# Kernel optimization log

Measured on AMD Instinct MI355X. Metric: run time of the kernel, lower is better.

Reference implementation:

```python
import jax, jax.numpy as jnp
import numpy as np

K = 3          # kernel size
STRIDE = 1
PAD = 1
DIL = 1
K2 = K * K


def setup_inputs() -> dict:
    key = jax.random.key(0)
    ks = jax.random.split(key, 5)
    B, Cin, Cout, H, W = 8, 128, 128, 64, 64
    x = jax.random.normal(ks[0], (B, Cin, H, W), jnp.float32)
    # conv_offset_mask: Conv2d(Cin, 3*dg*K*K=27, 3x3). Original inits to zero;
    # use small random weights so offsets are nonzero sub-pixel shifts.
    w_off = jax.random.normal(ks[1], (3 * K2, Cin, K, K), jnp.float32) * 0.05
    b_off = jax.random.normal(ks[2], (3 * K2,), jnp.float32) * 0.1
    weight = jax.random.normal(ks[3], (Cout, Cin, K, K), jnp.float32) / np.sqrt(Cin * K2)
    bias = jax.random.normal(ks[4], (Cout,), jnp.float32) * 0.1
    return dict(x=x, w_off=w_off, b_off=b_off, weight=weight, bias=bias)


def _conv(x, w, b):
    y = jax.lax.conv_general_dilated(
        x, w, (STRIDE, STRIDE), [(PAD, PAD), (PAD, PAD)],
        dimension_numbers=('NCHW', 'OIHW', 'NCHW'))
    return y + b[None, :, None, None]


def _sample_one(xb, pyb, pxb, mb):
    Cin, Hin, Win = xb.shape
    y0 = jnp.floor(pyb)
    x0 = jnp.floor(pxb)
    wy = pyb - y0   # fractional weights
    wx = pxb - x0
    y0i = y0.astype(jnp.int32)
    x0i = x0.astype(jnp.int32)
    xf = xb.reshape(Cin, -1)

    def g(yi, xi):
        valid = ((yi >= 0) & (yi < Hin) & (xi >= 0) & (xi < Win)).astype(xb.dtype)
        idx = jnp.clip(yi, 0, Hin - 1) * Win + jnp.clip(xi, 0, Win - 1)
        return xf[:, idx] * valid[None]   # [Cin,K2,Ho,Wo]

    v = (g(y0i, x0i) * ((1 - wy) * (1 - wx))[None]
         + g(y0i, x0i + 1) * ((1 - wy) * wx)[None]
         + g(y0i + 1, x0i) * (wy * (1 - wx))[None]
         + g(y0i + 1, x0i + 1) * (wy * wx)[None])
    return v * mb[None]   # modulated columns [Cin,K2,Ho,Wo]


def reference(x, w_off, b_off, weight, bias):
    B, Cin, Hin, Win = x.shape
    Cout = weight.shape[0]
    om = _conv(x, w_off, b_off)                 # [B, 3*K2, Ho, Wo]
    dy = om[:, :K2]
    dx = om[:, K2:2 * K2]
    m = jax.nn.sigmoid(om[:, 2 * K2:])          # modulation mask
    Ho, Wo = dy.shape[2], dy.shape[3]
    kh = jnp.repeat(jnp.arange(K), K)           # [K2] kernel row per tap
    kw = jnp.tile(jnp.arange(K), K)             # [K2] kernel col per tap
    grid_y = jnp.arange(Ho) * STRIDE - PAD
    grid_x = jnp.arange(Wo) * STRIDE - PAD
    py = dy + grid_y[None, None, :, None] + (kh * DIL)[None, :, None, None]
    px = dx + grid_x[None, None, None, :] + (kw * DIL)[None, :, None, None]
    cols = jax.vmap(_sample_one)(x, py, px, m)  # [B,Cin,K2,Ho,Wo]
    out = jnp.einsum('bckhw,ock->bohw', cols, weight.reshape(Cout, Cin, K2))
    return out + bias[None, :, None, None]
```

## Files before the change

kernel.cpp:

```cpp
#include <hip/hip_runtime.h>
#include <math.h>

#define BATCH 8
#define CIN   128
#define COUT  128
#define HH    64
#define WW    64
#define OC    27
#define KDIM  1152

typedef unsigned short u16;
typedef unsigned int   u32;
typedef __attribute__((ext_vector_type(8))) short bf16x8;
typedef __attribute__((ext_vector_type(4))) float f32x4;

__device__ __forceinline__ float b2f(u16 u) {
    return __uint_as_float((u32)u << 16);
}
__device__ __forceinline__ u16 f2b(float f) {
    u32 u = __float_as_uint(f);
    return (u16)((u + 0x7fffu + ((u >> 16) & 1u)) >> 16);
}
__device__ __forceinline__ float blo(u32 u) { return __uint_as_float(u << 16); }
__device__ __forceinline__ float bhi(u32 u) { return __uint_as_float(u & 0xffff0000u); }
__device__ __forceinline__ u32 cvtpk(float lo, float hi) {
    u32 r;
    asm("v_cvt_pk_bf16_f32 %0, %1, %2" : "=v"(r) : "v"(lo), "v"(hi));
    return r;
}

__device__ __forceinline__ int xswiz(int o, int K) { return (o & 7) * K + (o >> 3); }

__global__ __launch_bounds__(256) void k_prep(const float* __restrict__ x,
                                              const float* __restrict__ weight,
                                              const float* __restrict__ w_off,
                                              u16* __restrict__ xtb,
                                              u16* __restrict__ xlo,
                                              u16* __restrict__ wbf,
                                              u16* __restrict__ wop) {
    __shared__ float tile[64][65];
    int gbid = blockIdx.x;
    int t = threadIdx.x;
    if (gbid < 1024) {
        int bid = xswiz(gbid, 128);
        int b   = bid >> 7;
        int c0  = ((bid >> 6) & 1) << 6;
        int hw0 = (bid & 63) << 6;
        int ln  = t & 63;
        int cq  = t >> 6;
#pragma unroll
        for (int r = 0; r < 16; ++r) {
            int c_l = cq * 16 + r;
            tile[c_l][ln] = x[(((size_t)(b * CIN + c0 + c_l)) << 12) + hw0 + ln];
        }
        __syncthreads();
#pragma unroll
        for (int r = 0; r < 16; ++r) {
            int hw_w = cq * 16 + r;
            float v = tile[ln][hw_w];
            u16 hi = f2b(v);
            u16 lo = f2b(v - b2f(hi));
            size_t dst = ((size_t)(b << 12) + hw0 + hw_w) * 128 + c0 + ln;
            xtb[dst] = hi;
            xlo[dst] = lo;
        }
    } else if (gbid < 1600) {
        int tid = (gbid - 1024) * 256 + t;
        int j  = tid & 7;
        int l  = (tid >> 3) & 63;
        int ni = (tid >> 9) & 7;
        int s  = (tid >> 12) & 3;
        int t9 = tid >> 14;
        int co = ni * 16 + (l & 15);
        int ci = s * 32 + ((l >> 4) << 3) + j;
        wbf[tid] = f2b(weight[co * KDIM + ci * 9 + t9]);
    } else {
        int tid = (gbid - 1600) * 256 + t;
        int j   = tid & 7;
        int l   = (tid >> 3) & 63;
        int ni  = (tid >> 9) & 1;
        int sg  = (tid >> 10) & 3;
        int rest = tid >> 12;
        int t9  = rest % 9;
        int split = rest / 9;
        int co = ni * 16 + (l & 15);
        int ci = sg * 32 + ((l >> 4) << 3) + j;
        float val = (co < OC) ? w_off[co * KDIM + ci * 9 + t9] : 0.f;
        u16 hi = f2b(val);
        u16 lo = f2b(val - b2f(hi));
        wop[tid] = split ? lo : hi;
    }
}

__global__ __launch_bounds__(512, 4) void k_off_mfma(const u16* __restrict__ xtb,
                                                     const u16* __restrict__ xlo,
                                                     const u16* __restrict__ wop,
                                                     const float* __restrict__ b_off,
                                                     float* __restrict__ om) {
    __shared__ __align__(16) u16 Xh[3 * 66 * 64];
    __shared__ __align__(16) u16 Xl[3 * 66 * 64];
    __shared__ __align__(16) float red[4][32][16];

    const int t    = threadIdx.x;
    const int lb   = xswiz(blockIdx.x, 64);
    const int b    = lb >> 6;
    const int h    = lb & 63;
    const int tl   = t & 255;
    const int sgrp = t >> 8;
    const int l    = tl & 63;
    const int wv2  = tl >> 6;
    const int row0 = l & 15;
    const int kg   = l >> 4;

    f32x4 acc0 = {0.f, 0.f, 0.f, 0.f};
    f32x4 acc1 = {0.f, 0.f, 0.f, 0.f};

    bf16x8 vh_[4], vl_[4];
    const bf16x8 zero8 = {0, 0, 0, 0, 0, 0, 0, 0};

    auto stage_load = [&](int half) {
#pragma unroll
        for (int it = 0; it < 4; ++it) {
            int i = t + it * 512;
            vh_[it] = zero8;
            vl_[it] = zero8;
            if (i < 1584) {
                int row = i / 528;
                int rem = i - row * 528;
                int p = rem >> 3, q = rem & 7;
                int grow = h - 1 + row;
                int gw   = p - 1;
                if ((unsigned)grow < 64u && (unsigned)gw < 64u) {
                    size_t src = ((((size_t)b << 12) + (grow << 6) + gw) << 7) + half * 64 + q * 8;
                    vh_[it] = *(const bf16x8*)(xtb + src);
                    vl_[it] = *(const bf16x8*)(xlo + src);
                }
            }
        }
    };
    auto stage_store = [&]() {
#pragma unroll
        for (int it = 0; it < 4; ++it) {
            int i = t + it * 512;
            if (i < 1584) {
                int row = i / 528;
                int rem = i - row * 528;
                int p = rem >> 3, q = rem & 7;
                int dstb = ((row * 66 + p) << 7) + ((q ^ (p & 7)) << 4);
                *(bf16x8*)((char*)Xh + dstb) = vh_[it];
                *(bf16x8*)((char*)Xl + dstb) = vl_[it];
            }
        }
    };
    auto kloop = [&](int half) {
        for (int tap = 0; tap < 9; ++tap) {
            int kh = tap / 3, kw = tap - kh * 3;
            int p = wv2 * 16 + row0 + kw;
            int rowb = (kh * 66 + p) << 7;
            int q = sgrp * 4 + kg;
            int off = rowb + ((q ^ (p & 7)) << 4);
            bf16x8 ah = *(const bf16x8*)((const char*)Xh + off);
            bf16x8 al = *(const bf16x8*)((const char*)Xl + off);
            int sg = half * 2 + sgrp;
            const u16* B = wop + (((tap * 4 + sg)) << 10) + (l << 3);
            bf16x8 bh0 = *(const bf16x8*)(B);
            bf16x8 bh1 = *(const bf16x8*)(B + 512);
            bf16x8 bl0 = *(const bf16x8*)(B + 36864);
            bf16x8 bl1 = *(const bf16x8*)(B + 36864 + 512);
            acc0 = __builtin_amdgcn_mfma_f32_16x16x32_bf16(ah, bh0, acc0, 0, 0, 0);
            acc1 = __builtin_amdgcn_mfma_f32_16x16x32_bf16(ah, bh1, acc1, 0, 0, 0);
            acc0 = __builtin_amdgcn_mfma_f32_16x16x32_bf16(al, bh0, acc0, 0, 0, 0);
            acc1 = __builtin_amdgcn_mfma_f32_16x16x32_bf16(al, bh1, acc1, 0, 0, 0);
            acc0 = __builtin_amdgcn_mfma_f32_16x16x32_bf16(ah, bl0, acc0, 0, 0, 0);
            acc1 = __builtin_amdgcn_mfma_f32_16x16x32_bf16(ah, bl1, acc1, 0, 0, 0);
        }
    };

    stage_load(0);
    stage_store();
    __syncthreads();
    stage_load(1);
    kloop(0);
    __syncthreads();
    stage_store();
    __syncthreads();
    kloop(1);

    if (sgrp) {
        *(f32x4*)&red[wv2][row0][kg * 4]      = acc0;
        *(f32x4*)&red[wv2][row0 + 16][kg * 4] = acc1;
    }
    __syncthreads();
    if (!sgrp) {
        acc0 += *(const f32x4*)&red[wv2][row0][kg * 4];
        acc1 += *(const f32x4*)&red[wv2][row0 + 16][kg * 4];
        int wpx = wv2 * 16 + (kg << 2);
        int co0 = row0;
        {
            float bb = b_off[co0];
            float4 r = make_float4(acc0.x + bb, acc0.y + bb, acc0.z + bb, acc0.w + bb);
            *(float4*)(om + (((size_t)(b * OC + co0)) << 12) + (h << 6) + wpx) = r;
        }
        int co1 = co0 + 16;
        if (co1 < OC) {
            float bb = b_off[co1];
            float4 r = make_float4(acc1.x + bb, acc1.y + bb, acc1.z + bb, acc1.w + bb);
            if (co1 >= 18) {
                r.x = 1.f / (1.f + expf(-r.x));
                r.y = 1.f / (1.f + expf(-r.y));
                r.z = 1.f / (1.f + expf(-r.z));
                r.w = 1.f / (1.f + expf(-r.w));
            }
            *(float4*)(om + (((size_t)(b * OC + co1)) << 12) + (h << 6) + wpx) = r;
        }
    }
}

__global__ __launch_bounds__(512, 4) void k_sample_gemm(const u16* __restrict__ xtb,
                                                        const float* __restrict__ om,
                                                        const u16* __restrict__ wbf,
                                                        const float* __restrict__ bias,
                                                        float* __restrict__ out) {
    __shared__ __align__(16) u16 Abuf[2][64 * 128];
    __shared__ float w4[576][4];
    __shared__ int y0c[576], x0c[576], y1c[576], x1c[576];

    const int t  = threadIdx.x;
    const int lb = xswiz(blockIdx.x, 64);
    const int b  = lb >> 6;
    const int h  = lb & 63;

    for (int i = t; i < 576; i += 512) {
        int p  = i / 9;
        int tt = i - p * 9;
        const float* ob = om + ((size_t)b * OC) * 4096 + (h << 6) + p;
        float dy = ob[(size_t)tt << 12];
        float dx = ob[(size_t)(9 + tt) << 12];
        float m  = ob[(size_t)(18 + tt) << 12];
        float py = dy + (float)(h - 1 + tt / 3);
        float px = dx + (float)(p - 1 + tt % 3);
        float y0f = floorf(py), x0f = floorf(px);
        float wy = py - y0f, wx = px - x0f;
        int y0 = (int)y0f, x0 = (int)x0f;
        int y1 = y0 + 1,   x1 = x0 + 1;
        float vy0 = ((unsigned)y0 < 64u) ? 1.f : 0.f;
        float vy1 = ((unsigned)y1 < 64u) ? 1.f : 0.f;
        float vx0 = ((unsigned)x0 < 64u) ? 1.f : 0.f;
        float vx1 = ((unsigned)x1 < 64u) ? 1.f : 0.f;
        w4[i][0] = (1.f - wy) * (1.f - wx) * m * vy0 * vx0;
        w4[i][1] = (1.f - wy) * wx         * m * vy0 * vx1;
        w4[i][2] = wy         * (1.f - wx) * m * vy1 * vx0;
        w4[i][3] = wy         * wx         * m * vy1 * vx1;
        y0c[i] = min(max(y0, 0), 63);
        y1c[i] = min(max(y1, 0), 63);
        x0c[i] = min(max(x0, 0), 63);
        x1c[i] = min(max(x1, 0), 63);
    }
    __syncthreads();

    f32x4 acc[4][2];
#pragma unroll
    for (int pt = 0; pt < 4; ++pt)
#pragma unroll
        for (int nt = 0; nt < 2; ++nt) acc[pt][nt] = (f32x4){0.f, 0.f, 0.f, 0.f};

    const int grp  = t >> 8;
    const int tl   = t & 255;
    const int l    = tl & 63;
    const int wv2  = tl >> 6;
    const int row0 = l & 15;
    const int kg   = l >> 4;

    const int sp = tl >> 2;
    const int sc = tl & 3;
    const u16* xb = xtb + ((size_t)b << 19);

    uint4 g_[2][4];

    auto sample_load = [&](int tt) {
        int pi = sp * 9 + tt;
        int o00 = (((y0c[pi] << 6) | x0c[pi]) << 7) + grp * 64;
        int o01 = (((y0c[pi] << 6) | x1c[pi]) << 7) + grp * 64;
        int o10 = (((y1c[pi] << 6) | x0c[pi]) << 7) + grp * 64;
        int o11 = (((y1c[pi] << 6) | x1c[pi]) << 7) + grp * 64;
#pragma unroll
        for (int k = 0; k < 2; ++k) {
            int ch = k * 32 + sc * 8;
            g_[k][0] = *(const uint4*)(xb + o00 + ch);
            g_[k][1] = *(const uint4*)(xb + o01 + ch);
            g_[k][2] = *(const uint4*)(xb + o10 + ch);
            g_[k][3] = *(const uint4*)(xb + o11 + ch);
        }
    };

    auto sample_finish = [&](int tt, int buf) {
        int pi = sp * 9 + tt;
        float4 W = *(const float4*)(&w4[pi][0]);
        u16* dst = &Abuf[buf][0];
#pragma unroll
        for (int k = 0; k < 2; ++k) {
            uint4 a00 = g_[k][0], a01 = g_[k][1], a10 = g_[k][2], a11 = g_[k][3];
            uint4 ow;
            {
                float e0 = W.x * blo(a00.x) + W.y * blo(a01.x) + W.z * blo(a10.x) + W.w * blo(a11.x);
                float e1 = W.x * bhi(a00.x) + W.y * bhi(a01.x) + W.z * bhi(a10.x) + W.w * bhi(a11.x);
                ow.x = cvtpk(e0, e1);
            }
            {
                float e0 = W.x * blo(a00.y) + W.y * blo(a01.y) + W.z * blo(a10.y) + W.w * blo(a11.y);
                float e1 = W.x * bhi(a00.y) + W.y * bhi(a01.y) + W.z * bhi(a10.y) + W.w * bhi(a11.y);
                ow.y = cvtpk(e0, e1);
            }
            {
                float e0 = W.x * blo(a00.z) + W.y * blo(a01.z) + W.z * blo(a10.z) + W.w * blo(a11.z);
                float e1 = W.x * bhi(a00.z) + W.y * bhi(a01.z) + W.z * bhi(a10.z) + W.w * bhi(a11.z);
                ow.z = cvtpk(e0, e1);
            }
            {
                float e0 = W.x * blo(a00.w) + W.y * blo(a01.w) + W.z * blo(a10.w) + W.w * blo(a11.w);
                float e1 = W.x * bhi(a00.w) + W.y * bhi(a01.w) + W.z * bhi(a10.w) + W.w * bhi(a11.w);
                ow.w = cvtpk(e0, e1);
            }
            int q16 = (grp * 8 + k * 4 + sc) ^ (sp & 15);
            *(uint4*)((char*)dst + (sp << 8) + (q16 << 4)) = ow;
        }
    };

    auto domfma = [&](int t9, int buf) {
        const char* Ab = (const char*)&Abuf[buf][0];
#pragma unroll
        for (int shalf = 0; shalf < 2; ++shalf) {
            int s = grp * 2 + shalf;
            int q = s * 4 + kg;
            int sw = (q ^ row0) << 4;
            bf16x8 a[4];
#pragma unroll
            for (int pt = 0; pt < 4; ++pt)
                a[pt] = *(const bf16x8*)(Ab + ((pt * 16 + row0) << 8) + sw);
            const u16* B = wbf + ((size_t)t9 << 14) + (s << 12) + (wv2 << 10) + (l << 3);
            bf16x8 b0 = *(const bf16x8*)(B);
            bf16x8 b1 = *(const bf16x8*)(B + 512);
#pragma unroll
            for (int pt = 0; pt < 4; ++pt) {
                acc[pt][0] = __builtin_amdgcn_mfma_f32_16x16x32_bf16(a[pt], b0, acc[pt][0], 0, 0, 0);
                acc[pt][1] = __builtin_amdgcn_mfma_f32_16x16x32_bf16(a[pt], b1, acc[pt][1], 0, 0, 0);
            }
        }
    };

    sample_load(0);
    sample_finish(0, 0);
    __syncthreads();
    for (int tt = 0; tt < 9; ++tt) {
        if (tt < 8) sample_load(tt + 1);
        domfma(tt, tt & 1);
        if (tt < 8) sample_finish(tt + 1, (tt + 1) & 1);
        __syncthreads();
    }

    float* outs = (float*)&Abuf[0][0];
    if (grp) {
#pragma unroll
        for (int pt = 0; pt < 4; ++pt)
#pragma unroll
            for (int nt = 0; nt < 2; ++nt) {
                int co  = wv2 * 32 + nt * 16 + row0;
                int pxq = pt * 4 + kg;
                *(f32x4*)((char*)outs + (co << 8) + ((pxq ^ (co & 7)) << 4)) = acc[pt][nt];
            }
    }
    __syncthreads();
    if (!grp) {
#pragma unroll
        for (int pt = 0; pt < 4; ++pt)
#pragma unroll
            for (int nt = 0; nt < 2; ++nt) {
                int co  = wv2 * 32 + nt * 16 + row0;
                int pxq = pt * 4 + kg;
                char* ad = (char*)outs + (co << 8) + ((pxq ^ (co & 7)) << 4);
                f32x4 v = *(const f32x4*)ad;
                *(f32x4*)ad = v + acc[pt][nt];
            }
    }
    __syncthreads();
    {
        int co = t >> 2, qt = t & 3;
        float bb = bias[co];
        float* og = out + (((size_t)(b * COUT + co)) << 12) + (h << 6);
#pragma unroll
        for (int j = 0; j < 4; ++j) {
            int pxq = qt * 4 + j;
            f32x4 v = *(const f32x4*)((const char*)outs + (co << 8) + ((pxq ^ (co & 7)) << 4));
            float4 r = make_float4(v.x + bb, v.y + bb, v.z + bb, v.w + bb);
            *reinterpret_cast<float4*>(og + pxq * 4) = r;
        }
    }
}

extern "C" void kernel_launch(void* const* d_in, const int* in_sizes, int n_in,
                              void* d_out, int out_size, void* d_ws, size_t ws_size,
                              hipStream_t stream) {
    const float* x      = (const float*)d_in[0];
    const float* w_off  = (const float*)d_in[1];
    const float* b_off  = (const float*)d_in[2];
    const float* weight = (const float*)d_in[3];
    const float* bias   = (const float*)d_in[4];
    float* out = (float*)d_out;

    float* om  = (float*)d_ws;
    u16*   xtb = (u16*)(om + 884736);
    u16*   wbf = xtb + 4194304;
    u16*   wop = wbf + 147456;
    u16*   xlo = (u16*)d_out;

    k_prep<<<1888, 256, 0, stream>>>(x, weight, w_off, xtb, xlo, wbf, wop);
    k_off_mfma<<<512, 512, 0, stream>>>(xtb, xlo, wop, b_off, om);
    k_sample_gemm<<<512, 512, 0, stream>>>(xtb, om, wbf, bias, out);
}
```

Baseline: 56.31 us.

## Fuse offset conv into sample-GEMM kernel, computing hi/lo bf16 split on the fly

Merges the offset/mask convolution kernel into the deformable sampling GEMM kernel. The per-row offsets stay in shared memory instead of making a round trip through a global workspace. The offset conv now stages raw fp32 x rows into LDS and forms the bf16 hi/lo split per MFMA operand, so the prep kernel no longer writes the xlo array. This removes a kernel launch and the global traffic for om and xlo. In exchange it uses more LDS per block (about 72KB), which may reduce occupancy, and adds conversion ALU work inside the offset conv loop.

```diff
diff --git a/kernel.cpp b/kernel.cpp
--- a/kernel.cpp
+++ b/kernel.cpp
@@ -28,6 +28,11 @@
     asm("v_cvt_pk_bf16_f32 %0, %1, %2" : "=v"(r) : "v"(lo), "v"(hi));
     return r;
 }
+__device__ __forceinline__ bf16x8 pack8(u32 a, u32 b, u32 c, u32 d) {
+    union { u32 u[4]; bf16x8 v; } z;
+    z.u[0] = a; z.u[1] = b; z.u[2] = c; z.u[3] = d;
+    return z.v;
+}
 
 __device__ __forceinline__ int xswiz(int o, int K) { return (o & 7) * K + (o >> 3); }
 
@@ -35,7 +40,6 @@
                                               const float* __restrict__ weight,
                                               const float* __restrict__ w_off,
                                               u16* __restrict__ xtb,
-                                              u16* __restrict__ xlo,
                                               u16* __restrict__ wbf,
                                               u16* __restrict__ wop) {
     __shared__ float tile[64][65];
@@ -57,12 +61,7 @@
 #pragma unroll
         for (int r = 0; r < 16; ++r) {
             int hw_w = cq * 16 + r;
-            float v = tile[ln][hw_w];
-            u16 hi = f2b(v);
-            u16 lo = f2b(v - b2f(hi));
-            size_t dst = ((size_t)(b << 12) + hw0 + hw_w) * 128 + c0 + ln;
-            xtb[dst] = hi;
-            xlo[dst] = lo;
+            xtb[((size_t)(b << 12) + hw0 + hw_w) * 128 + c0 + ln] = f2b(tile[ln][hw_w]);
         }
     } else if (gbid < 1600) {
         int tid = (gbid - 1024) * 256 + t;
@@ -92,151 +91,151 @@
     }
 }
 
-__global__ __launch_bounds__(512, 4) void k_off_mfma(const u16* __restrict__ xtb,
-                                                     const u16* __restrict__ xlo,
-                                                     const u16* __restrict__ wop,
-                                                     const float* __restrict__ b_off,
-                                                     float* __restrict__ om) {
-    __shared__ __align__(16) u16 Xh[3 * 66 * 64];
-    __shared__ __align__(16) u16 Xl[3 * 66 * 64];
-    __shared__ __align__(16) float red[4][32][16];
-
-    const int t    = threadIdx.x;
-    const int lb   = xswiz(blockIdx.x, 64);
-    const int b    = lb >> 6;
-    const int h    = lb & 63;
-    const int tl   = t & 255;
-    const int sgrp = t >> 8;
-    const int l    = tl & 63;
-    const int wv2  = tl >> 6;
-    const int row0 = l & 15;
-    const int kg   = l >> 4;
-
-    f32x4 acc0 = {0.f, 0.f, 0.f, 0.f};
-    f32x4 acc1 = {0.f, 0.f, 0.f, 0.f};
-
-    bf16x8 vh_[4], vl_[4];
-    const bf16x8 zero8 = {0, 0, 0, 0, 0, 0, 0, 0};
-
-    auto stage_load = [&](int half) {
-#pragma unroll
-        for (int it = 0; it < 4; ++it) {
-            int i = t + it * 512;
-            vh_[it] = zero8;
-            vl_[it] = zero8;
-            if (i < 1584) {
-                int row = i / 528;
-                int rem = i - row * 528;
-                int p = rem >> 3, q = rem & 7;
-                int grow = h - 1 + row;
-                int gw   = p - 1;
-                if ((unsigned)grow < 64u && (unsigned)gw < 64u) {
-                    size_t src = ((((size_t)b << 12) + (grow << 6) + gw) << 7) + half * 64 + q * 8;
-                    vh_[it] = *(const bf16x8*)(xtb + src);
-                    vl_[it] = *(const bf16x8*)(xlo + src);
-                }
-            }
-        }
-    };
-    auto stage_store = [&]() {
-#pragma unroll
-        for (int it = 0; it < 4; ++it) {
-            int i = t + it * 512;
-            if (i < 1584) {
-                int row = i / 528;
-                int rem = i - row * 528;
-                int p = rem >> 3, q = rem & 7;
-                int dstb = ((row * 66 + p) << 7) + ((q ^ (p & 7)) << 4);
-                *(bf16x8*)((char*)Xh + dstb) = vh_[it];
-                *(bf16x8*)((char*)Xl + dstb) = vl_[it];
-            }
-        }
-    };
-    auto kloop = [&](int half) {
-        for (int tap = 0; tap < 9; ++tap) {
-            int kh = tap / 3, kw = tap - kh * 3;
-            int p = wv2 * 16 + row0 + kw;
-            int rowb = (kh * 66 + p) << 7;
-            int q = sgrp * 4 + kg;
-            int off = rowb + ((q ^ (p & 7)) << 4);
-            bf16x8 ah = *(const bf16x8*)((const char*)Xh + off);
-            bf16x8 al = *(const bf16x8*)((const char*)Xl + off);
-            int sg = half * 2 + sgrp;
-            const u16* B = wop + (((tap * 4 + sg)) << 10) + (l << 3);
-            bf16x8 bh0 = *(const bf16x8*)(B);
-            bf16x8 bh1 = *(const bf16x8*)(B + 512);
-            bf16x8 bl0 = *(const bf16x8*)(B + 36864);
-            bf16x8 bl1 = *(const bf16x8*)(B + 36864 + 512);
-            acc0 = __builtin_amdgcn_mfma_f32_16x16x32_bf16(ah, bh0, acc0, 0, 0, 0);
-            acc1 = __builtin_amdgcn_mfma_f32_16x16x32_bf16(ah, bh1, acc1, 0, 0, 0);
-            acc0 = __builtin_amdgcn_mfma_f32_16x16x32_bf16(al, bh0, acc0, 0, 0, 0);
-            acc1 = __builtin_amdgcn_mfma_f32_16x16x32_bf16(al, bh1, acc1, 0, 0, 0);
-            acc0 = __builtin_amdgcn_mfma_f32_16x16x32_bf16(ah, bl0, acc0, 0, 0, 0);
-            acc1 = __builtin_amdgcn_mfma_f32_16x16x32_bf16(ah, bl1, acc1, 0, 0, 0);
-        }
-    };
-
-    stage_load(0);
-    stage_store();
-    __syncthreads();
-    stage_load(1);
-    kloop(0);
-    __syncthreads();
-    stage_store();
-    __syncthreads();
-    kloop(1);
-
-    if (sgrp) {
-        *(f32x4*)&red[wv2][row0][kg * 4]      = acc0;
-        *(f32x4*)&red[wv2][row0 + 16][kg * 4] = acc1;
-    }
-    __syncthreads();
-    if (!sgrp) {
-        acc0 += *(const f32x4*)&red[wv2][row0][kg * 4];
-        acc1 += *(const f32x4*)&red[wv2][row0 + 16][kg * 4];
-        int wpx = wv2 * 16 + (kg << 2);
-        int co0 = row0;
-        {
-            float bb = b_off[co0];
-            float4 r = make_float4(acc0.x + bb, acc0.y + bb, acc0.z + bb, acc0.w + bb);
-            *(float4*)(om + (((size_t)(b * OC + co0)) << 12) + (h << 6) + wpx) = r;
-        }
-        int co1 = co0 + 16;
-        if (co1 < OC) {
-            float bb = b_off[co1];
-            float4 r = make_float4(acc1.x + bb, acc1.y + bb, acc1.z + bb, acc1.w + bb);
-            if (co1 >= 18) {
-                r.x = 1.f / (1.f + expf(-r.x));
-                r.y = 1.f / (1.f + expf(-r.y));
-                r.z = 1.f / (1.f + expf(-r.z));
-                r.w = 1.f / (1.f + expf(-r.w));
-            }
-            *(float4*)(om + (((size_t)(b * OC + co1)) << 12) + (h << 6) + wpx) = r;
-        }
-    }
-}
-
-__global__ __launch_bounds__(512, 4) void k_sample_gemm(const u16* __restrict__ xtb,
-                                                        const float* __restrict__ om,
-                                                        const u16* __restrict__ wbf,
-                                                        const float* __restrict__ bias,
-                                                        float* __restrict__ out) {
-    __shared__ __align__(16) u16 Abuf[2][64 * 128];
-    __shared__ float w4[576][4];
-    __shared__ int y0c[576], x0c[576], y1c[576], x1c[576];
+#define CST 228
+__global__ __launch_bounds__(512, 4) void k_fused(const float* __restrict__ x,
+                                                  const u16* __restrict__ xtb,
+                                                  const u16* __restrict__ wop,
+                                                  const u16* __restrict__ wbf,
+                                                  const float* __restrict__ b_off,
+                                                  const float* __restrict__ bias,
+                                                  float* __restrict__ out) {
+    __shared__ __align__(16) char smem[73472];
+    float* Xf  = (float*)smem;
+    float* red = (float*)(smem + 58368);
+    float* omf = (float*)(smem + 66560);
 
     const int t  = threadIdx.x;
     const int lb = xswiz(blockIdx.x, 64);
     const int b  = lb >> 6;
     const int h  = lb & 63;
+    const int l    = t & 63;
+    const int wv   = t >> 6;
+    const int l15  = l & 15;
+    const int lg   = l >> 4;
+
+    {
+        const int ntile = wv & 3;
+        const int kgrp  = wv >> 2;
+
+        if (t < 192) {
+            int ci = t & 63, row = t >> 6;
+            int idx = ci * CST + row * 68 + (((ci >> 3) & 3) << 3) + 64;
+            *(float4*)(Xf + idx) = make_float4(0.f, 0.f, 0.f, 0.f);
+        }
+
+        f32x4 acc0 = {0.f, 0.f, 0.f, 0.f};
+        f32x4 acc1 = {0.f, 0.f, 0.f, 0.f};
+        float4 st_[6];
+
+        auto stageA_load = [&](int half) {
+#pragma unroll
+            for (int it = 0; it < 6; ++it) {
+                int slot = t + it * 512;
+                int pair = slot >> 4, ln16 = slot & 15;
+                int row = pair >> 6, ci = pair & 63;
+                int grow = h - 1 + row;
+                float4 v = make_float4(0.f, 0.f, 0.f, 0.f);
+                if ((unsigned)grow < 64u)
+                    v = *(const float4*)(x + (((size_t)(b * CIN + half * 64 + ci)) << 12)
+                                           + (grow << 6) + ln16 * 4);
+                st_[it] = v;
+            }
+        };
+        auto stageA_store = [&]() {
+#pragma unroll
+            for (int it = 0; it < 6; ++it) {
+                int slot = t + it * 512;
+                int pair = slot >> 4, ln16 = slot & 15;
+                int row = pair >> 6, ci = pair & 63;
+                int idx = ci * CST + row * 68 + (((ci >> 3) & 3) << 3) + ln16 * 4;
+                *(float4*)(Xf + idx) = st_[it];
+            }
+        };
+        auto kloopA = [&](int half) {
+            for (int tap = 0; tap < 9; ++tap) {
+                int kh = tap / 3, kw = tap - kh * 3;
+                int gw = ntile * 16 + kw - 1 + l15;
+                int px = (gw < 0) ? 64 : ((gw > 63) ? 65 : gw);
+                int ci0 = kgrp * 32 + (lg << 3);
+                int base = ci0 * CST + kh * 68 + (((ci0 >> 3) & 3) << 3) + px;
+                float f0 = Xf[base], f1 = Xf[base + CST];
+                float f2 = Xf[base + 2 * CST], f3 = Xf[base + 3 * CST];
+                float f4 = Xf[base + 4 * CST], f5 = Xf[base + 5 * CST];
+                float f6 = Xf[base + 6 * CST], f7 = Xf[base + 7 * CST];
+                u32 h0 = cvtpk(f0, f1), h1 = cvtpk(f2, f3);
+                u32 h2 = cvtpk(f4, f5), h3 = cvtpk(f6, f7);
+                u32 l0 = cvtpk(f0 - blo(h0), f1 - bhi(h0));
+                u32 l1 = cvtpk(f2 - blo(h1), f3 - bhi(h1));
+                u32 l2 = cvtpk(f4 - blo(h2), f5 - bhi(h2));
+                u32 l3 = cvtpk(f6 - blo(h3), f7 - bhi(h3));
+                bf16x8 ah = pack8(h0, h1, h2, h3);
+                bf16x8 al = pack8(l0, l1, l2, l3);
+                int sg = half * 2 + kgrp;
+                const u16* B = wop + (((tap * 4 + sg) * 2) << 9) + (l << 3);
+                bf16x8 wh0 = *(const bf16x8*)(B);
+                bf16x8 wh1 = *(const bf16x8*)(B + 512);
+                bf16x8 wl0 = *(const bf16x8*)(B + 36864);
+                bf16x8 wl1 = *(const bf16x8*)(B + 36864 + 512);
+                acc0 = __builtin_amdgcn_mfma_f32_16x16x32_bf16(wh0, ah, acc0, 0, 0, 0);
+                acc1 = __builtin_amdgcn_mfma_f32_16x16x32_bf16(wh1, ah, acc1, 0, 0, 0);
+                acc0 = __builtin_amdgcn_mfma_f32_16x16x32_bf16(wl0, ah, acc0, 0, 0, 0);
+                acc1 = __builtin_amdgcn_mfma_f32_16x16x32_bf16(wl1, ah, acc1, 0, 0, 0);
+                acc0 = __builtin_amdgcn_mfma_f32_16x16x32_bf16(wh0, al, acc0, 0, 0, 0);
+                acc1 = __builtin_amdgcn_mfma_f32_16x16x32_bf16(wh1, al, acc1, 0, 0, 0);
+            }
+        };
+
+        stageA_load(0);
+        stageA_store();
+        __syncthreads();
+        stageA_load(1);
+        kloopA(0);
+        __syncthreads();
+        stageA_store();
+        __syncthreads();
+        kloopA(1);
+
+        if (kgrp) {
+            float* rp = red + (((ntile << 6) + l) << 3);
+            *(f32x4*)rp = acc0;
+            *(f32x4*)(rp + 4) = acc1;
+        }
+        __syncthreads();
+        if (!kgrp) {
+            const float* rp = red + (((ntile << 6) + l) << 3);
+            acc0 += *(const f32x4*)rp;
+            acc1 += *(const f32x4*)(rp + 4);
+            int px = ntile * 16 + l15;
+            int co0 = lg << 2;
+#pragma unroll
+            for (int r = 0; r < 4; ++r)
+                omf[((co0 + r) << 6) + px] = acc0[r] + b_off[co0 + r];
+            int co1 = 16 + (lg << 2);
+#pragma unroll
+            for (int r = 0; r < 4; ++r) {
+                int co = co1 + r;
+                if (co < OC) {
+                    float v = acc1[r] + b_off[co];
+                    if (co >= 18) v = 1.f / (1.f + expf(-v));
+                    omf[(co << 6) + px] = v;
+                }
+            }
+        }
+        __syncthreads();
+    }
+
+    float (*w4)[4] = (float (*)[4])(smem + 32768);
+    int* y0c = (int*)(smem + 41984);
+    int* x0c = (int*)(smem + 44288);
+    int* y1c = (int*)(smem + 46592);
+    int* x1c = (int*)(smem + 48896);
 
     for (int i = t; i < 576; i += 512) {
         int p  = i / 9;
         int tt = i - p * 9;
-        const float* ob = om + ((size_t)b * OC) * 4096 + (h << 6) + p;
-        float dy = ob[(size_t)tt << 12];
-        float dx = ob[(size_t)(9 + tt) << 12];
-        float m  = ob[(size_t)(18 + tt) << 12];
+        float dy = omf[(tt << 6) + p];
+        float dx = omf[((9 + tt) << 6) + p];
+        float m  = omf[((18 + tt) << 6) + p];
         float py = dy + (float)(h - 1 + tt / 3);
         float px = dx + (float)(p - 1 + tt % 3);
         float y0f = floorf(py), x0f = floorf(px);
@@ -266,10 +265,10 @@
 
     const int grp  = t >> 8;
     const int tl   = t & 255;
-    const int l    = tl & 63;
+    const int l2   = tl & 63;
     const int wv2  = tl >> 6;
-    const int row0 = l & 15;
-    const int kg   = l >> 4;
+    const int row0 = l2 & 15;
+    const int kg   = l2 >> 4;
 
     const int sp = tl >> 2;
     const int sc = tl & 3;
@@ -296,7 +295,7 @@
     auto sample_finish = [&](int tt, int buf) {
         int pi = sp * 9 + tt;
         float4 W = *(const float4*)(&w4[pi][0]);
-        u16* dst = &Abuf[buf][0];
+        u16* dst = (u16*)(smem + buf * 16384);
 #pragma unroll
         for (int k = 0; k < 2; ++k) {
             uint4 a00 = g_[k][0], a01 = g_[k][1], a10 = g_[k][2], a11 = g_[k][3];
@@ -327,7 +326,7 @@
     };
 
     auto domfma = [&](int t9, int buf) {
-        const char* Ab = (const char*)&Abuf[buf][0];
+        const char* Ab = (const char*)(smem + buf * 16384);
 #pragma unroll
         for (int shalf = 0; shalf < 2; ++shalf) {
             int s = grp * 2 + shalf;
@@ -337,7 +336,7 @@
 #pragma unroll
             for (int pt = 0; pt < 4; ++pt)
                 a[pt] = *(const bf16x8*)(Ab + ((pt * 16 + row0) << 8) + sw);
-            const u16* B = wbf + ((size_t)t9 << 14) + (s << 12) + (wv2 << 10) + (l << 3);
+            const u16* B = wbf + ((size_t)t9 << 14) + (s << 12) + (wv2 << 10) + (l2 << 3);
             bf16x8 b0 = *(const bf16x8*)(B);
             bf16x8 b1 = *(const bf16x8*)(B + 512);
 #pragma unroll
@@ -358,7 +357,7 @@
         __syncthreads();
     }
 
-    float* outs = (float*)&Abuf[0][0];
+    float* outs = (float*)smem;
     if (grp) {
 #pragma unroll
         for (int pt = 0; pt < 4; ++pt)
@@ -407,13 +406,10 @@
     const float* bias   = (const float*)d_in[4];
     float* out = (float*)d_out;
 
-    float* om  = (float*)d_ws;
-    u16*   xtb = (u16*)(om + 884736);
-    u16*   wbf = xtb + 4194304;
-    u16*   wop = wbf + 147456;
-    u16*   xlo = (u16*)d_out;
-
-    k_prep<<<1888, 256, 0, stream>>>(x, weight, w_off, xtb, xlo, wbf, wop);
-    k_off_mfma<<<512, 512, 0, stream>>>(xtb, xlo, wop, b_off, om);
-    k_sample_gemm<<<512, 512, 0, stream>>>(xtb, om, wbf, bias, out);
-}
+    u16* xtb = (u16*)d_ws;
+    u16* wbf = xtb + 4194304;
+    u16* wop = wbf + 147456;
+
+    k_prep<<<1888, 256, 0, stream>>>(x, weight, w_off, xtb, wbf, wop);
+    k_fused<<<512, 512, 0, stream>>>(x, xtb, wop, wbf, b_off, bias, out);
+}
```

After: 48.35 us. 14.1% less time.
